# Performance work log

Measured on AMD Instinct MI355X. Metric: run time of the kernel, lower is better.

The kernel has to match this reference:

```python
import jax, jax.numpy as jnp
import numpy as np

B = 8
FEAT = 256
HID = 256
NCLS = 80
SIZES = [(128, 128), (64, 64), (32, 32), (16, 16), (8, 8)]
DELTA_XY = 0.1   # dd_delta_range_xy
DELTA_WH = 2.0   # dd_delta_range_wh
PRIOR_P = 0.01   # prior_cls_prob


def _priors():
    # prior_cxcy: normalized grid centers per pyramid level (sine_pos_encodings id maps,
    # normalize=True with all-ones masks). prior_wh: (1/fW, 1/fH) per level.
    cxcy, wh = [], []
    for (h, w) in SIZES:
        cy = (jnp.arange(h, dtype=jnp.float32) + 0.5) / h
        cx = (jnp.arange(w, dtype=jnp.float32) + 0.5) / w
        gx, gy = jnp.meshgrid(cx, cy, indexing='xy')           # [h, w]
        cxcy.append(jnp.stack([gx, gy], axis=-1).reshape(h * w, 2))
        wh.append(jnp.broadcast_to(jnp.array([1.0 / w, 1.0 / h], jnp.float32), (h * w, 2)))
    return jnp.concatenate(cxcy, axis=0), jnp.concatenate(wh, axis=0)  # [N,2], [N,2]


def _mlp(x, Wh, bh, Wo, bo):
    # Linear(feat->hidden) + ReLU, then Linear(hidden->out)
    h = jax.nn.relu(jnp.einsum('bnf,hf->bnh', x, Wh) + bh)
    return jnp.einsum('bnh,oh->bno', h, Wo) + bo


def setup_inputs() -> dict:
    key = jax.random.key(0)
    ks = jax.random.split(key, 12)
    inp = {}
    for i, (h, w) in enumerate(SIZES):
        inp[f'fm{i}'] = jax.random.normal(ks[i], (B, FEAT, h, w), dtype=jnp.float32)
    s_in = 1.0 / np.sqrt(FEAT)
    s_h = 1.0 / np.sqrt(HID)
    bias_value = float(-np.log((1.0 - PRIOR_P) / PRIOR_P))
    inp['cls_Wh'] = jax.random.normal(ks[5], (HID, FEAT), dtype=jnp.float32) * s_in
    inp['cls_bh'] = jnp.zeros((HID,), jnp.float32)
    inp['cls_Wo'] = jax.random.normal(ks[6], (NCLS, HID), dtype=jnp.float32) * s_h
    inp['cls_bo'] = jnp.full((NCLS,), bias_value, jnp.float32)  # focal prior bias init
    inp['box_Wh'] = jax.random.normal(ks[7], (HID, FEAT), dtype=jnp.float32) * s_in
    inp['box_bh'] = jnp.zeros((HID,), jnp.float32)
    inp['box_Wo'] = jax.random.normal(ks[8], (4, HID), dtype=jnp.float32) * s_h
    inp['box_bo'] = jnp.zeros((4,), jnp.float32)  # zero-init box bias
    return inp


def reference(fm0, fm1, fm2, fm3, fm4,
              cls_Wh, cls_bh, cls_Wo, cls_bo,
              box_Wh, box_bh, box_Wo, box_bo):
    fms = [fm0, fm1, fm2, fm3, fm4]
    # obj_feats: concat of flatten(2).permute(0,2,1) -> [B, N, FEAT]
    obj_feats = jnp.concatenate(
        [f.reshape(B, FEAT, -1).transpose(0, 2, 1) for f in fms], axis=1)
    cls_logits = _mlp(obj_feats, cls_Wh, cls_bh, cls_Wo, cls_bo)   # [B, N, NCLS]
    box_logits = _mlp(obj_feats, box_Wh, box_bh, box_Wo, box_bo)   # [B, N, 4]
    box_deltas = jnp.tanh(box_logits)
    prior_cxcy, prior_wh = _priors()
    pred_cxcy = prior_cxcy[None] + DELTA_XY * box_deltas[:, :, :2]
    pred_wh = prior_wh[None] * (DELTA_WH ** box_deltas[:, :, 2:])
    # pack [cls_logits | pred_boxes(cxcywh)] -> [B, N, NCLS+4]
    return jnp.concatenate([cls_logits, pred_cxcy, pred_wh], axis=-1)
```

## Files before the change

kernel.cpp:

```cpp
#include <hip/hip_runtime.h>
#include <hip/hip_bf16.h>
#include <math.h>
#include <stdint.h>

#define NTOK 21824

typedef __attribute__((ext_vector_type(8)))  short bf16x8;
typedef __attribute__((ext_vector_type(4)))  float f32x4;
typedef __attribute__((ext_vector_type(16))) float f32x16;

__device__ __forceinline__ uint32_t f2bf(float f) {
    uint32_t u = __builtin_bit_cast(uint32_t, f);
    return (u + 0x7FFFu + ((u >> 16) & 1u)) >> 16;
}
__device__ __forceinline__ uint32_t pkbf2(float lo, float hi) {
    __hip_bfloat162 h = __float22bfloat162_rn(float2{lo, hi});
    uint32_t r; __builtin_memcpy(&r, &h, 4);
    return r;
}

#define WOFF_CWH 0
#define WOFF_BWH 65536
#define WOFF_CWO 131072
#define WOFF_BWO 151552

__global__ void prep_weights(const float* __restrict__ cWh, const float* __restrict__ cWo,
                             const float* __restrict__ bWh, const float* __restrict__ bWo,
                             uint16_t* __restrict__ ws) {
    int i = blockIdx.x * 256 + threadIdx.x;
    if (i >= 155648) return;
    uint32_t v;
    if (i < 65536)       v = f2bf(cWh[i]);
    else if (i < 131072) v = f2bf(bWh[i - 65536]);
    else if (i < 151552) v = f2bf(cWo[i - 131072]);
    else { int j = i - 151552; v = (j < 1024) ? f2bf(bWo[j]) : 0u; }
    ws[i] = (uint16_t)v;
}

__global__ __launch_bounds__(512, 4) void dfd_fused(
    const float* __restrict__ fm0, const float* __restrict__ fm1,
    const float* __restrict__ fm2, const float* __restrict__ fm3,
    const float* __restrict__ fm4,
    const float* __restrict__ cls_bh, const float* __restrict__ cls_bo,
    const float* __restrict__ box_bh, const float* __restrict__ box_bo,
    const uint16_t* __restrict__ wbf,
    float* __restrict__ out)
{
    __shared__ uint16_t LB[64 * 512];
    uint16_t* Xs = LB;
    uint16_t* Hs = LB;

    const int tid  = threadIdx.x;
    const int lane = tid & 63;
    const int w    = tid >> 6;
    const int r    = lane & 15;
    const int q    = lane >> 4;
    const int col  = lane & 31;
    const int hi   = lane >> 5;
    const int n0   = blockIdx.x * 64;
    const int b    = blockIdx.y;

    const float* fm; int off, ls;
    if      (n0 < 16384) { fm = fm0; off = 0;     ls = 7; }
    else if (n0 < 20480) { fm = fm1; off = 16384; ls = 6; }
    else if (n0 < 21504) { fm = fm2; off = 20480; ls = 5; }
    else if (n0 < 21760) { fm = fm3; off = 21504; ls = 4; }
    else                 { fm = fm4; off = 21760; ls = 3; }
    const int dim = 1 << ls;
    const int hw  = dim * dim;
    const int p0  = n0 - off;

    {
        const int t  = lane;
        const int sw = (t & 7) << 3;
        const float* src = fm + (size_t)b * 256 * hw + p0 + t;
        #pragma unroll
        for (int i = 0; i < 4; ++i) {
            const int f0 = w * 8 + i * 64;
            float x[8];
            #pragma unroll
            for (int e = 0; e < 8; ++e) x[e] = src[(size_t)(f0 + e) * hw];
            uint4 pk;
            pk.x = pkbf2(x[0], x[1]); pk.y = pkbf2(x[2], x[3]);
            pk.z = pkbf2(x[4], x[5]); pk.w = pkbf2(x[6], x[7]);
            *reinterpret_cast<uint4*>(&Xs[t * 256 + (f0 ^ sw)]) = pk;
        }
    }
    __syncthreads();

    f32x16 acc[2][2];
    {
        #pragma unroll
        for (int mt = 0; mt < 2; ++mt)
            #pragma unroll
            for (int nt = 0; nt < 2; ++nt)
                #pragma unroll
                for (int e = 0; e < 16; ++e) acc[mt][nt][e] = 0.f;

        const int hh0 = w * 64;
        const uint16_t* Wbase = (w < 4) ? wbf + WOFF_CWH + hh0 * 256
                                        : wbf + WOFF_BWH + (hh0 - 256) * 256;
        const int kh = hi * 8;
        const uint16_t* Wr = Wbase + col * 256 + kh;
        const int sw0 = (col & 7) << 3;

        #pragma unroll
        for (int ks = 0; ks < 16; ++ks) {
            const bf16x8 a0 = *(const bf16x8*)(Wr + ks * 16);
            const bf16x8 a1 = *(const bf16x8*)(Wr + 8192 + ks * 16);
            const int kx = (ks * 16 + kh) ^ sw0;
            const bf16x8 x0 = *(const bf16x8*)&Xs[col * 256 + kx];
            const bf16x8 x1 = *(const bf16x8*)&Xs[(32 + col) * 256 + kx];
            acc[0][0] = __builtin_amdgcn_mfma_f32_32x32x16_bf16(a0, x0, acc[0][0], 0, 0, 0);
            acc[0][1] = __builtin_amdgcn_mfma_f32_32x32x16_bf16(a0, x1, acc[0][1], 0, 0, 0);
            acc[1][0] = __builtin_amdgcn_mfma_f32_32x32x16_bf16(a1, x0, acc[1][0], 0, 0, 0);
            acc[1][1] = __builtin_amdgcn_mfma_f32_32x32x16_bf16(a1, x1, acc[1][1], 0, 0, 0);
        }
    }
    __syncthreads();

    {
        const int hh0 = w * 64;
        const float* bh_ = (w < 4) ? cls_bh + hh0 : box_bh + (hh0 - 256);
        #pragma unroll
        for (int mt = 0; mt < 2; ++mt) {
            #pragma unroll
            for (int nt = 0; nt < 2; ++nt) {
                const int t   = nt * 32 + col;
                const int swt = (t & 7) << 3;
                #pragma unroll
                for (int g = 0; g < 4; ++g) {
                    const int hb = mt * 32 + 8 * g + 4 * hi;
                    const f32x4 bv = *(const f32x4*)(bh_ + hb);
                    const float v0 = fmaxf(acc[mt][nt][4 * g + 0] + bv[0], 0.f);
                    const float v1 = fmaxf(acc[mt][nt][4 * g + 1] + bv[1], 0.f);
                    const float v2 = fmaxf(acc[mt][nt][4 * g + 2] + bv[2], 0.f);
                    const float v3 = fmaxf(acc[mt][nt][4 * g + 3] + bv[3], 0.f);
                    uint2 pk; pk.x = pkbf2(v0, v1); pk.y = pkbf2(v2, v3);
                    *reinterpret_cast<uint2*>(&Hs[t * 512 + ((hh0 + hb) ^ swt)]) = pk;
                }
            }
        }
    }
    __syncthreads();

    if (w < 5) {
        f32x4 c[4];
        #pragma unroll
        for (int m = 0; m < 4; ++m) c[m] = {0.f, 0.f, 0.f, 0.f};
        const uint16_t* Bw = wbf + WOFF_CWO + (w * 16 + r) * 256 + q * 8;
        #pragma unroll
        for (int kq = 0; kq < 8; ++kq) {
            const bf16x8 bfr = *(const bf16x8*)(Bw + kq * 32);
            #pragma unroll
            for (int m = 0; m < 4; ++m) {
                const int t = m * 16 + r;
                const int kcol = (kq * 32 + q * 8) ^ ((t & 7) << 3);
                const bf16x8 a = *(const bf16x8*)&Hs[t * 512 + kcol];
                c[m] = __builtin_amdgcn_mfma_f32_16x16x32_bf16(a, bfr, c[m], 0, 0, 0);
            }
        }
        const float bo_l = cls_bo[w * 16 + r];
        #pragma unroll
        for (int m = 0; m < 4; ++m)
            #pragma unroll
            for (int jj = 0; jj < 4; ++jj)
                out[((size_t)b * NTOK + n0 + m * 16 + q * 4 + jj) * 84 + w * 16 + r]
                    = c[m][jj] + bo_l;
    } else if (w < 7) {
        const int m0 = (w - 5) * 2;
        f32x4 c[2];
        c[0] = {0.f, 0.f, 0.f, 0.f}; c[1] = {0.f, 0.f, 0.f, 0.f};
        const uint16_t* Bw = wbf + WOFF_BWO + r * 256 + q * 8;
        #pragma unroll
        for (int kq = 0; kq < 8; ++kq) {
            const bf16x8 bfr = *(const bf16x8*)(Bw + kq * 32);
            #pragma unroll
            for (int mm = 0; mm < 2; ++mm) {
                const int t = (m0 + mm) * 16 + r;
                const int kcol = 256 + ((kq * 32 + q * 8) ^ ((t & 7) << 3));
                const bf16x8 a = *(const bf16x8*)&Hs[t * 512 + kcol];
                c[mm] = __builtin_amdgcn_mfma_f32_16x16x32_bf16(a, bfr, c[mm], 0, 0, 0);
            }
        }
        if (r < 4) {
            const float bo_l = box_bo[r];
            const float inv  = 1.0f / (float)dim;
            #pragma unroll
            for (int mm = 0; mm < 2; ++mm)
                #pragma unroll
                for (int jj = 0; jj < 4; ++jj) {
                    const int t = (m0 + mm) * 16 + q * 4 + jj;
                    const int p = p0 + t;
                    const float d = tanhf(c[mm][jj] + bo_l);
                    float val;
                    if (r == 0)      val = ((float)(p & (dim - 1)) + 0.5f) * inv + 0.1f * d;
                    else if (r == 1) val = ((float)(p >> ls) + 0.5f) * inv + 0.1f * d;
                    else             val = exp2f(d) * inv;
                    out[((size_t)b * NTOK + n0 + t) * 84 + 80 + r] = val;
                }
        }
    }
}

extern "C" void kernel_launch(void* const* d_in, const int* in_sizes, int n_in,
                              void* d_out, int out_size, void* d_ws, size_t ws_size,
                              hipStream_t stream) {
    uint16_t* ws = (uint16_t*)d_ws;
    prep_weights<<<608, 256, 0, stream>>>(
        (const float*)d_in[5],  (const float*)d_in[7],
        (const float*)d_in[9],  (const float*)d_in[11], ws);
    dim3 grid(NTOK / 64, 8);
    dfd_fused<<<grid, 512, 0, stream>>>(
        (const float*)d_in[0], (const float*)d_in[1], (const float*)d_in[2],
        (const float*)d_in[3], (const float*)d_in[4],
        (const float*)d_in[6],  (const float*)d_in[8],
        (const float*)d_in[10], (const float*)d_in[12],
        ws, (float*)d_out);
}
```

Measured before the change: 135.7 us.

## Split fused MLP into two kernels with bf16 hidden buffer in workspace

```diff
diff --git a/kernel.cpp b/kernel.cpp
--- a/kernel.cpp
+++ b/kernel.cpp
@@ -23,6 +23,7 @@
 #define WOFF_BWH 65536
 #define WOFF_CWO 131072
 #define WOFF_BWO 151552
+#define HID_OFF  155648
 
 __global__ void prep_weights(const float* __restrict__ cWh, const float* __restrict__ cWo,
                              const float* __restrict__ bWh, const float* __restrict__ bWo,
@@ -35,6 +36,178 @@
     else if (i < 151552) v = f2bf(cWo[i - 131072]);
     else { int j = i - 151552; v = (j < 1024) ? f2bf(bWo[j]) : 0u; }
     ws[i] = (uint16_t)v;
+}
+
+__device__ __forceinline__ void level_lookup(
+    int n0, const float* fm0, const float* fm1, const float* fm2,
+    const float* fm3, const float* fm4, const float*& fm, int& off, int& ls) {
+    if      (n0 < 16384) { fm = fm0; off = 0;     ls = 7; }
+    else if (n0 < 20480) { fm = fm1; off = 16384; ls = 6; }
+    else if (n0 < 21504) { fm = fm2; off = 20480; ls = 5; }
+    else if (n0 < 21760) { fm = fm3; off = 21504; ls = 4; }
+    else                 { fm = fm4; off = 21760; ls = 3; }
+}
+
+__global__ __launch_bounds__(512, 4) void dfd_g1(
+    const float* __restrict__ fm0, const float* __restrict__ fm1,
+    const float* __restrict__ fm2, const float* __restrict__ fm3,
+    const float* __restrict__ fm4,
+    const float* __restrict__ cls_bh, const float* __restrict__ box_bh,
+    const uint16_t* __restrict__ wbf,
+    uint16_t* __restrict__ hid,
+    int b0)
+{
+    __shared__ uint16_t Xs[64 * 256];
+
+    const int tid  = threadIdx.x;
+    const int lane = tid & 63;
+    const int w    = tid >> 6;
+    const int col  = lane & 31;
+    const int hi   = lane >> 5;
+    const int n0   = blockIdx.x * 64;
+    const int lb   = blockIdx.y;
+    const int b    = b0 + lb;
+
+    const float* fm; int off, ls;
+    level_lookup(n0, fm0, fm1, fm2, fm3, fm4, fm, off, ls);
+    const int hw = 1 << (2 * ls);
+    const int p0 = n0 - off;
+
+    {
+        const int t  = lane;
+        const int sw = (t & 7) << 3;
+        const float* src = fm + (size_t)b * 256 * hw + p0 + t;
+        #pragma unroll
+        for (int i = 0; i < 4; ++i) {
+            const int f0 = w * 8 + i * 64;
+            float x[8];
+            #pragma unroll
+            for (int e = 0; e < 8; ++e) x[e] = src[(size_t)(f0 + e) * hw];
+            uint4 pk;
+            pk.x = pkbf2(x[0], x[1]); pk.y = pkbf2(x[2], x[3]);
+            pk.z = pkbf2(x[4], x[5]); pk.w = pkbf2(x[6], x[7]);
+            *reinterpret_cast<uint4*>(&Xs[t * 256 + (f0 ^ sw)]) = pk;
+        }
+    }
+    __syncthreads();
+
+    f32x16 acc[2][2];
+    #pragma unroll
+    for (int mt = 0; mt < 2; ++mt)
+        #pragma unroll
+        for (int nt = 0; nt < 2; ++nt)
+            #pragma unroll
+            for (int e = 0; e < 16; ++e) acc[mt][nt][e] = 0.f;
+
+    const int hh0 = w * 64;
+    const uint16_t* Wbase = (w < 4) ? wbf + WOFF_CWH + hh0 * 256
+                                    : wbf + WOFF_BWH + (hh0 - 256) * 256;
+    const int kh = hi * 8;
+    const uint16_t* Wr = Wbase + col * 256 + kh;
+    const int sw0 = (col & 7) << 3;
+
+    #pragma unroll
+    for (int ks = 0; ks < 16; ++ks) {
+        const bf16x8 a0 = *(const bf16x8*)(Wr + ks * 16);
+        const bf16x8 a1 = *(const bf16x8*)(Wr + 8192 + ks * 16);
+        const int kx = (ks * 16 + kh) ^ sw0;
+        const bf16x8 x0 = *(const bf16x8*)&Xs[col * 256 + kx];
+        const bf16x8 x1 = *(const bf16x8*)&Xs[(32 + col) * 256 + kx];
+        acc[0][0] = __builtin_amdgcn_mfma_f32_32x32x16_bf16(a0, x0, acc[0][0], 0, 0, 0);
+        acc[0][1] = __builtin_amdgcn_mfma_f32_32x32x16_bf16(a0, x1, acc[0][1], 0, 0, 0);
+        acc[1][0] = __builtin_amdgcn_mfma_f32_32x32x16_bf16(a1, x0, acc[1][0], 0, 0, 0);
+        acc[1][1] = __builtin_amdgcn_mfma_f32_32x32x16_bf16(a1, x1, acc[1][1], 0, 0, 0);
+    }
+
+    const float* bh_ = (w < 4) ? cls_bh + hh0 : box_bh + (hh0 - 256);
+    #pragma unroll
+    for (int nt = 0; nt < 2; ++nt) {
+        const int t = nt * 32 + col;
+        uint16_t* hrow = hid + ((size_t)lb * NTOK + n0 + t) * 512 + hh0;
+        #pragma unroll
+        for (int mt = 0; mt < 2; ++mt) {
+            #pragma unroll
+            for (int g = 0; g < 4; ++g) {
+                const int hb = mt * 32 + 8 * g + 4 * hi;
+                const f32x4 bv = *(const f32x4*)(bh_ + hb);
+                const float v0 = fmaxf(acc[mt][nt][4 * g + 0] + bv[0], 0.f);
+                const float v1 = fmaxf(acc[mt][nt][4 * g + 1] + bv[1], 0.f);
+                const float v2 = fmaxf(acc[mt][nt][4 * g + 2] + bv[2], 0.f);
+                const float v3 = fmaxf(acc[mt][nt][4 * g + 3] + bv[3], 0.f);
+                uint2 pk; pk.x = pkbf2(v0, v1); pk.y = pkbf2(v2, v3);
+                *reinterpret_cast<uint2*>(hrow + hb) = pk;
+            }
+        }
+    }
+}
+
+__global__ __launch_bounds__(256, 6) void dfd_g2(
+    const float* __restrict__ cls_bo, const float* __restrict__ box_bo,
+    const uint16_t* __restrict__ wbf,
+    const uint16_t* __restrict__ hid,
+    float* __restrict__ out,
+    int b0)
+{
+    const int tid  = threadIdx.x;
+    const int lane = tid & 63;
+    const int w    = tid >> 6;
+    const int r    = lane & 15;
+    const int q    = lane >> 4;
+    const int n0   = blockIdx.x * 64;
+    const int lb   = blockIdx.y;
+    const int b    = b0 + lb;
+    const int t0   = n0 + w * 16;
+
+    int off, ls; const float* fm_unused;
+    level_lookup(n0, nullptr, nullptr, nullptr, nullptr, nullptr, fm_unused, off, ls);
+    const int dim = 1 << ls;
+    const int p0  = n0 - off;
+
+    f32x4 c[6];
+    #pragma unroll
+    for (int m = 0; m < 6; ++m) c[m] = {0.f, 0.f, 0.f, 0.f};
+
+    const uint16_t* hrow = hid + ((size_t)lb * NTOK + t0 + r) * 512 + q * 8;
+    const uint16_t* WoA  = wbf + WOFF_CWO + r * 256 + q * 8;
+    const uint16_t* WoB  = wbf + WOFF_BWO + r * 256 + q * 8;
+
+    #pragma unroll
+    for (int kq = 0; kq < 8; ++kq) {
+        const bf16x8 hbc = *(const bf16x8*)(hrow + kq * 32);
+        const bf16x8 hbb = *(const bf16x8*)(hrow + 256 + kq * 32);
+        #pragma unroll
+        for (int m = 0; m < 5; ++m) {
+            const bf16x8 a = *(const bf16x8*)(WoA + m * 4096 + kq * 32);
+            c[m] = __builtin_amdgcn_mfma_f32_16x16x32_bf16(a, hbc, c[m], 0, 0, 0);
+        }
+        const bf16x8 ab = *(const bf16x8*)(WoB + kq * 32);
+        c[5] = __builtin_amdgcn_mfma_f32_16x16x32_bf16(ab, hbb, c[5], 0, 0, 0);
+    }
+
+    float* orow = out + ((size_t)b * NTOK + t0 + r) * 84;
+    #pragma unroll
+    for (int m = 0; m < 5; ++m) {
+        const f32x4 bo = *(const f32x4*)(cls_bo + m * 16 + q * 4);
+        f32x4 v;
+        #pragma unroll
+        for (int jj = 0; jj < 4; ++jj) v[jj] = c[m][jj] + bo[jj];
+        *(f32x4*)(orow + m * 16 + q * 4) = v;
+    }
+    if (q == 0) {
+        const f32x4 bo = *(const f32x4*)box_bo;
+        const float inv = 1.0f / (float)dim;
+        const int p = p0 + w * 16 + r;
+        const float d0 = tanhf(c[5][0] + bo[0]);
+        const float d1 = tanhf(c[5][1] + bo[1]);
+        const float d2 = tanhf(c[5][2] + bo[2]);
+        const float d3 = tanhf(c[5][3] + bo[3]);
+        f32x4 v;
+        v[0] = ((float)(p & (dim - 1)) + 0.5f) * inv + 0.1f * d0;
+        v[1] = ((float)(p >> ls) + 0.5f) * inv + 0.1f * d1;
+        v[2] = exp2f(d2) * inv;
+        v[3] = exp2f(d3) * inv;
+        *(f32x4*)(orow + 80) = v;
+    }
 }
 
 __global__ __launch_bounds__(512, 4) void dfd_fused(
@@ -61,13 +234,9 @@
     const int b    = blockIdx.y;
 
     const float* fm; int off, ls;
-    if      (n0 < 16384) { fm = fm0; off = 0;     ls = 7; }
-    else if (n0 < 20480) { fm = fm1; off = 16384; ls = 6; }
-    else if (n0 < 21504) { fm = fm2; off = 20480; ls = 5; }
-    else if (n0 < 21760) { fm = fm3; off = 21504; ls = 4; }
-    else                 { fm = fm4; off = 21760; ls = 3; }
+    level_lookup(n0, fm0, fm1, fm2, fm3, fm4, fm, off, ls);
     const int dim = 1 << ls;
-    const int hw  = dim * dim;
+    const int hw  = 1 << (2 * ls);
     const int p0  = n0 - off;
 
     {
@@ -210,11 +379,34 @@
     prep_weights<<<608, 256, 0, stream>>>(
         (const float*)d_in[5],  (const float*)d_in[7],
         (const float*)d_in[9],  (const float*)d_in[11], ws);
-    dim3 grid(NTOK / 64, 8);
-    dfd_fused<<<grid, 512, 0, stream>>>(
-        (const float*)d_in[0], (const float*)d_in[1], (const float*)d_in[2],
-        (const float*)d_in[3], (const float*)d_in[4],
-        (const float*)d_in[6],  (const float*)d_in[8],
-        (const float*)d_in[10], (const float*)d_in[12],
-        ws, (float*)d_out);
-}
+
+    const size_t HID_B_PER_BATCH = (size_t)NTOK * 512 * 2;
+    const size_t W_BYTES = (size_t)HID_OFF * 2;
+    int nb = 0;
+    if      (ws_size >= W_BYTES + 4 * HID_B_PER_BATCH) nb = 4;
+    else if (ws_size >= W_BYTES + 2 * HID_B_PER_BATCH) nb = 2;
+    else if (ws_size >= W_BYTES + 1 * HID_B_PER_BATCH) nb = 1;
+
+    if (nb > 0) {
+        uint16_t* hid = ws + HID_OFF;
+        for (int b0 = 0; b0 < 8; b0 += nb) {
+            dim3 g(NTOK / 64, nb);
+            dfd_g1<<<g, 512, 0, stream>>>(
+                (const float*)d_in[0], (const float*)d_in[1], (const float*)d_in[2],
+                (const float*)d_in[3], (const float*)d_in[4],
+                (const float*)d_in[6], (const float*)d_in[10],
+                ws, hid, b0);
+            dfd_g2<<<g, 256, 0, stream>>>(
+                (const float*)d_in[8], (const float*)d_in[12],
+                ws, hid, (float*)d_out, b0);
+        }
+    } else {
+        dim3 grid(NTOK / 64, 8);
+        dfd_fused<<<grid, 512, 0, stream>>>(
+            (const float*)d_in[0], (const float*)d_in[1], (const float*)d_in[2],
+            (const float*)d_in[3], (const float*)d_in[4],
+            (const float*)d_in[6],  (const float*)d_in[8],
+            (const float*)d_in[10], (const float*)d_in[12],
+            ws, (float*)d_out);
+    }
+}
```

After: 290.6 us (median of 2 runs). 2.14x slower.

## Halve token tile to 32 with 4-wave blocks and rebalance second-layer work

Applied to the files above, without the earlier changes.

```diff
diff --git a/kernel.cpp b/kernel.cpp
--- a/kernel.cpp
+++ b/kernel.cpp
@@ -37,7 +37,7 @@
     ws[i] = (uint16_t)v;
 }
 
-__global__ __launch_bounds__(512, 4) void dfd_fused(
+__global__ __launch_bounds__(256, 4) void dfd_fused(
     const float* __restrict__ fm0, const float* __restrict__ fm1,
     const float* __restrict__ fm2, const float* __restrict__ fm3,
     const float* __restrict__ fm4,
@@ -46,7 +46,7 @@
     const uint16_t* __restrict__ wbf,
     float* __restrict__ out)
 {
-    __shared__ uint16_t LB[64 * 512];
+    __shared__ uint16_t LB[32 * 512];
     uint16_t* Xs = LB;
     uint16_t* Hs = LB;
 
@@ -57,7 +57,7 @@
     const int q    = lane >> 4;
     const int col  = lane & 31;
     const int hi   = lane >> 5;
-    const int n0   = blockIdx.x * 64;
+    const int n0   = blockIdx.x * 32;
     const int b    = blockIdx.y;
 
     const float* fm; int off, ls;
@@ -67,16 +67,17 @@
     else if (n0 < 21760) { fm = fm3; off = 21504; ls = 4; }
     else                 { fm = fm4; off = 21760; ls = 3; }
     const int dim = 1 << ls;
-    const int hw  = dim * dim;
+    const int hw  = 1 << (2 * ls);
     const int p0  = n0 - off;
 
     {
-        const int t  = lane;
+        const int t  = tid & 31;
+        const int fg = tid >> 5;
         const int sw = (t & 7) << 3;
         const float* src = fm + (size_t)b * 256 * hw + p0 + t;
         #pragma unroll
         for (int i = 0; i < 4; ++i) {
-            const int f0 = w * 8 + i * 64;
+            const int f0 = fg * 32 + i * 8;
             float x[8];
             #pragma unroll
             for (int e = 0; e < 8; ++e) x[e] = src[(size_t)(f0 + e) * hw];
@@ -88,117 +89,110 @@
     }
     __syncthreads();
 
-    f32x16 acc[2][2];
-    {
-        #pragma unroll
-        for (int mt = 0; mt < 2; ++mt)
-            #pragma unroll
-            for (int nt = 0; nt < 2; ++nt)
-                #pragma unroll
-                for (int e = 0; e < 16; ++e) acc[mt][nt][e] = 0.f;
-
-        const int hh0 = w * 64;
-        const uint16_t* Wbase = (w < 4) ? wbf + WOFF_CWH + hh0 * 256
-                                        : wbf + WOFF_BWH + (hh0 - 256) * 256;
+    f32x16 acc[4];
+    {
+        #pragma unroll
+        for (int mt = 0; mt < 4; ++mt)
+            #pragma unroll
+            for (int e = 0; e < 16; ++e) acc[mt][e] = 0.f;
+
+        const uint16_t* Wbase = (w < 2) ? wbf + WOFF_CWH + (w * 128) * 256
+                                        : wbf + WOFF_BWH + ((w - 2) * 128) * 256;
         const int kh = hi * 8;
         const uint16_t* Wr = Wbase + col * 256 + kh;
         const int sw0 = (col & 7) << 3;
 
         #pragma unroll
         for (int ks = 0; ks < 16; ++ks) {
-            const bf16x8 a0 = *(const bf16x8*)(Wr + ks * 16);
-            const bf16x8 a1 = *(const bf16x8*)(Wr + 8192 + ks * 16);
             const int kx = (ks * 16 + kh) ^ sw0;
             const bf16x8 x0 = *(const bf16x8*)&Xs[col * 256 + kx];
-            const bf16x8 x1 = *(const bf16x8*)&Xs[(32 + col) * 256 + kx];
-            acc[0][0] = __builtin_amdgcn_mfma_f32_32x32x16_bf16(a0, x0, acc[0][0], 0, 0, 0);
-            acc[0][1] = __builtin_amdgcn_mfma_f32_32x32x16_bf16(a0, x1, acc[0][1], 0, 0, 0);
-            acc[1][0] = __builtin_amdgcn_mfma_f32_32x32x16_bf16(a1, x0, acc[1][0], 0, 0, 0);
-            acc[1][1] = __builtin_amdgcn_mfma_f32_32x32x16_bf16(a1, x1, acc[1][1], 0, 0, 0);
+            #pragma unroll
+            for (int mt = 0; mt < 4; ++mt) {
+                const bf16x8 a = *(const bf16x8*)(Wr + mt * 8192 + ks * 16);
+                acc[mt] = __builtin_amdgcn_mfma_f32_32x32x16_bf16(a, x0, acc[mt], 0, 0, 0);
+            }
         }
     }
     __syncthreads();
 
     {
-        const int hh0 = w * 64;
-        const float* bh_ = (w < 4) ? cls_bh + hh0 : box_bh + (hh0 - 256);
-        #pragma unroll
-        for (int mt = 0; mt < 2; ++mt) {
-            #pragma unroll
-            for (int nt = 0; nt < 2; ++nt) {
-                const int t   = nt * 32 + col;
-                const int swt = (t & 7) << 3;
+        const float* bh_ = (w < 2) ? cls_bh + w * 128 : box_bh + (w - 2) * 128;
+        const int t   = col;
+        const int swt = (t & 7) << 3;
+        #pragma unroll
+        for (int mt = 0; mt < 4; ++mt) {
+            #pragma unroll
+            for (int g = 0; g < 4; ++g) {
+                const int hb = mt * 32 + 8 * g + 4 * hi;
+                const f32x4 bv = *(const f32x4*)(bh_ + hb);
+                const float v0 = fmaxf(acc[mt][4 * g + 0] + bv[0], 0.f);
+                const float v1 = fmaxf(acc[mt][4 * g + 1] + bv[1], 0.f);
+                const float v2 = fmaxf(acc[mt][4 * g + 2] + bv[2], 0.f);
+                const float v3 = fmaxf(acc[mt][4 * g + 3] + bv[3], 0.f);
+                uint2 pk; pk.x = pkbf2(v0, v1); pk.y = pkbf2(v2, v3);
+                *reinterpret_cast<uint2*>(&Hs[t * 512 + ((w * 128 + hb) ^ swt)]) = pk;
+            }
+        }
+    }
+    __syncthreads();
+
+    {
+        const int th = w & 1;
+        const int ms = w >> 1;
+        const int t  = th * 16 + r;
+        const int swt = (r & 7) << 3;
+        const uint16_t* hrow = &Hs[t * 512];
+        const int m0 = ms * 3;
+
+        f32x4 c[3];
+        c[0] = {0.f,0.f,0.f,0.f}; c[1] = {0.f,0.f,0.f,0.f}; c[2] = {0.f,0.f,0.f,0.f};
+        const uint16_t* WoA = wbf + WOFF_CWO + r * 256 + q * 8;
+        const uint16_t* WoB = wbf + WOFF_BWO + r * 256 + q * 8;
+
+        #pragma unroll
+        for (int kq = 0; kq < 8; ++kq) {
+            const int kcol = (kq * 32 + q * 8) ^ swt;
+            const bf16x8 a = *(const bf16x8*)&hrow[kcol];
+            const bf16x8 b0 = *(const bf16x8*)(WoA + (m0 + 0) * 4096 + kq * 32);
+            const bf16x8 b1 = *(const bf16x8*)(WoA + (m0 + 1) * 4096 + kq * 32);
+            c[0] = __builtin_amdgcn_mfma_f32_16x16x32_bf16(a, b0, c[0], 0, 0, 0);
+            c[1] = __builtin_amdgcn_mfma_f32_16x16x32_bf16(a, b1, c[1], 0, 0, 0);
+            if (ms == 0) {
+                const bf16x8 b2 = *(const bf16x8*)(WoA + 2 * 4096 + kq * 32);
+                c[2] = __builtin_amdgcn_mfma_f32_16x16x32_bf16(a, b2, c[2], 0, 0, 0);
+            } else {
+                const bf16x8 ab = *(const bf16x8*)&hrow[256 + kcol];
+                const bf16x8 b2 = *(const bf16x8*)(WoB + kq * 32);
+                c[2] = __builtin_amdgcn_mfma_f32_16x16x32_bf16(ab, b2, c[2], 0, 0, 0);
+            }
+        }
+
+        const int ncls = (ms == 0) ? 3 : 2;
+        #pragma unroll
+        for (int i = 0; i < 3; ++i) {
+            if (i < ncls) {
+                const int m = m0 + i;
+                const float bo_l = cls_bo[m * 16 + r];
                 #pragma unroll
-                for (int g = 0; g < 4; ++g) {
-                    const int hb = mt * 32 + 8 * g + 4 * hi;
-                    const f32x4 bv = *(const f32x4*)(bh_ + hb);
-                    const float v0 = fmaxf(acc[mt][nt][4 * g + 0] + bv[0], 0.f);
-                    const float v1 = fmaxf(acc[mt][nt][4 * g + 1] + bv[1], 0.f);
-                    const float v2 = fmaxf(acc[mt][nt][4 * g + 2] + bv[2], 0.f);
-                    const float v3 = fmaxf(acc[mt][nt][4 * g + 3] + bv[3], 0.f);
-                    uint2 pk; pk.x = pkbf2(v0, v1); pk.y = pkbf2(v2, v3);
-                    *reinterpret_cast<uint2*>(&Hs[t * 512 + ((hh0 + hb) ^ swt)]) = pk;
-                }
-            }
-        }
-    }
-    __syncthreads();
-
-    if (w < 5) {
-        f32x4 c[4];
-        #pragma unroll
-        for (int m = 0; m < 4; ++m) c[m] = {0.f, 0.f, 0.f, 0.f};
-        const uint16_t* Bw = wbf + WOFF_CWO + (w * 16 + r) * 256 + q * 8;
-        #pragma unroll
-        for (int kq = 0; kq < 8; ++kq) {
-            const bf16x8 bfr = *(const bf16x8*)(Bw + kq * 32);
-            #pragma unroll
-            for (int m = 0; m < 4; ++m) {
-                const int t = m * 16 + r;
-                const int kcol = (kq * 32 + q * 8) ^ ((t & 7) << 3);
-                const bf16x8 a = *(const bf16x8*)&Hs[t * 512 + kcol];
-                c[m] = __builtin_amdgcn_mfma_f32_16x16x32_bf16(a, bfr, c[m], 0, 0, 0);
-            }
-        }
-        const float bo_l = cls_bo[w * 16 + r];
-        #pragma unroll
-        for (int m = 0; m < 4; ++m)
-            #pragma unroll
-            for (int jj = 0; jj < 4; ++jj)
-                out[((size_t)b * NTOK + n0 + m * 16 + q * 4 + jj) * 84 + w * 16 + r]
-                    = c[m][jj] + bo_l;
-    } else if (w < 7) {
-        const int m0 = (w - 5) * 2;
-        f32x4 c[2];
-        c[0] = {0.f, 0.f, 0.f, 0.f}; c[1] = {0.f, 0.f, 0.f, 0.f};
-        const uint16_t* Bw = wbf + WOFF_BWO + r * 256 + q * 8;
-        #pragma unroll
-        for (int kq = 0; kq < 8; ++kq) {
-            const bf16x8 bfr = *(const bf16x8*)(Bw + kq * 32);
-            #pragma unroll
-            for (int mm = 0; mm < 2; ++mm) {
-                const int t = (m0 + mm) * 16 + r;
-                const int kcol = 256 + ((kq * 32 + q * 8) ^ ((t & 7) << 3));
-                const bf16x8 a = *(const bf16x8*)&Hs[t * 512 + kcol];
-                c[mm] = __builtin_amdgcn_mfma_f32_16x16x32_bf16(a, bfr, c[mm], 0, 0, 0);
-            }
-        }
-        if (r < 4) {
+                for (int jj = 0; jj < 4; ++jj)
+                    out[((size_t)b * NTOK + n0 + th * 16 + q * 4 + jj) * 84 + m * 16 + r]
+                        = c[i][jj] + bo_l;
+            }
+        }
+        if (ms == 1 && r < 4) {
             const float bo_l = box_bo[r];
             const float inv  = 1.0f / (float)dim;
             #pragma unroll
-            for (int mm = 0; mm < 2; ++mm)
-                #pragma unroll
-                for (int jj = 0; jj < 4; ++jj) {
-                    const int t = (m0 + mm) * 16 + q * 4 + jj;
-                    const int p = p0 + t;
-                    const float d = tanhf(c[mm][jj] + bo_l);
-                    float val;
-                    if (r == 0)      val = ((float)(p & (dim - 1)) + 0.5f) * inv + 0.1f * d;
-                    else if (r == 1) val = ((float)(p >> ls) + 0.5f) * inv + 0.1f * d;
-                    else             val = exp2f(d) * inv;
-                    out[((size_t)b * NTOK + n0 + t) * 84 + 80 + r] = val;
-                }
+            for (int jj = 0; jj < 4; ++jj) {
+                const int t2 = th * 16 + q * 4 + jj;
+                const int p  = p0 + t2;
+                const float d = tanhf(c[2][jj] + bo_l);
+                float val;
+                if (r == 0)      val = ((float)(p & (dim - 1)) + 0.5f) * inv + 0.1f * d;
+                else if (r == 1) val = ((float)(p >> ls) + 0.5f) * inv + 0.1f * d;
+                else             val = exp2f(d) * inv;
+                out[((size_t)b * NTOK + n0 + t2) * 84 + 80 + r] = val;
+            }
         }
     }
 }
@@ -210,8 +204,8 @@
     prep_weights<<<608, 256, 0, stream>>>(
         (const float*)d_in[5],  (const float*)d_in[7],
         (const float*)d_in[9],  (const float*)d_in[11], ws);
-    dim3 grid(NTOK / 64, 8);
-    dfd_fused<<<grid, 512, 0, stream>>>(
+    dim3 grid(NTOK / 32, 8);
+    dfd_fused<<<grid, 256, 0, stream>>>(
         (const float*)d_in[0], (const float*)d_in[1], (const float*)d_in[2],
         (const float*)d_in[3], (const float*)d_in[4],
         (const float*)d_in[6],  (const float*)d_in[8],
```

Result: slower. 263.2 us (+94.0%).

## Split cls and box heads across blocks with 128-token tiles

Applied to the files above, without the earlier changes.

```diff
diff --git a/kernel.cpp b/kernel.cpp
--- a/kernel.cpp
+++ b/kernel.cpp
@@ -4,6 +4,7 @@
 #include <stdint.h>
 
 #define NTOK 21824
+#define NTILE128 171
 
 typedef __attribute__((ext_vector_type(8)))  short bf16x8;
 typedef __attribute__((ext_vector_type(4)))  float f32x4;
@@ -37,7 +38,7 @@
     ws[i] = (uint16_t)v;
 }
 
-__global__ __launch_bounds__(512, 4) void dfd_fused(
+__global__ __launch_bounds__(512, 4) void dfd_head(
     const float* __restrict__ fm0, const float* __restrict__ fm1,
     const float* __restrict__ fm2, const float* __restrict__ fm3,
     const float* __restrict__ fm4,
@@ -46,7 +47,13 @@
     const uint16_t* __restrict__ wbf,
     float* __restrict__ out)
 {
-    __shared__ uint16_t LB[64 * 512];
+    const int g    = blockIdx.x;
+    const int s    = g & 15;
+    const int tile = (g >> 4) * 8 + (s & 7);
+    const int head = s >> 3;
+    if (tile >= NTILE128) return;
+
+    __shared__ uint16_t LB[128 * 256];
     uint16_t* Xs = LB;
     uint16_t* Hs = LB;
 
@@ -57,7 +64,7 @@
     const int q    = lane >> 4;
     const int col  = lane & 31;
     const int hi   = lane >> 5;
-    const int n0   = blockIdx.x * 64;
+    const int n0   = tile * 128;
     const int b    = blockIdx.y;
 
     const float* fm; int off, ls;
@@ -67,138 +74,134 @@
     else if (n0 < 21760) { fm = fm3; off = 21504; ls = 4; }
     else                 { fm = fm4; off = 21760; ls = 3; }
     const int dim = 1 << ls;
-    const int hw  = dim * dim;
+    const int hw  = 1 << (2 * ls);
     const int p0  = n0 - off;
+    const int T   = (n0 == 21760) ? 64 : 128;
+    const int NT16 = T >> 4;
 
     {
-        const int t  = lane;
+        const int t  = tid & 127;
+        const int fg = tid >> 7;
         const int sw = (t & 7) << 3;
-        const float* src = fm + (size_t)b * 256 * hw + p0 + t;
-        #pragma unroll
-        for (int i = 0; i < 4; ++i) {
-            const int f0 = w * 8 + i * 64;
-            float x[8];
-            #pragma unroll
-            for (int e = 0; e < 8; ++e) x[e] = src[(size_t)(f0 + e) * hw];
-            uint4 pk;
-            pk.x = pkbf2(x[0], x[1]); pk.y = pkbf2(x[2], x[3]);
-            pk.z = pkbf2(x[4], x[5]); pk.w = pkbf2(x[6], x[7]);
-            *reinterpret_cast<uint4*>(&Xs[t * 256 + (f0 ^ sw)]) = pk;
+        if (t < T) {
+            const float* src = fm + (size_t)b * 256 * hw + p0 + t;
+            #pragma unroll
+            for (int i = 0; i < 8; ++i) {
+                const int f0 = fg * 64 + i * 8;
+                float x[8];
+                #pragma unroll
+                for (int e = 0; e < 8; ++e) x[e] = src[(size_t)(f0 + e) * hw];
+                uint4 pk;
+                pk.x = pkbf2(x[0], x[1]); pk.y = pkbf2(x[2], x[3]);
+                pk.z = pkbf2(x[4], x[5]); pk.w = pkbf2(x[6], x[7]);
+                *reinterpret_cast<uint4*>(&Xs[t * 256 + (f0 ^ sw)]) = pk;
+            }
         }
     }
     __syncthreads();
 
-    f32x16 acc[2][2];
+    f32x16 acc[4];
     {
         #pragma unroll
-        for (int mt = 0; mt < 2; ++mt)
-            #pragma unroll
-            for (int nt = 0; nt < 2; ++nt)
-                #pragma unroll
-                for (int e = 0; e < 16; ++e) acc[mt][nt][e] = 0.f;
-
-        const int hh0 = w * 64;
-        const uint16_t* Wbase = (w < 4) ? wbf + WOFF_CWH + hh0 * 256
-                                        : wbf + WOFF_BWH + (hh0 - 256) * 256;
+        for (int nt = 0; nt < 4; ++nt)
+            #pragma unroll
+            for (int e = 0; e < 16; ++e) acc[nt][e] = 0.f;
+
+        const int hhw = w * 32;
+        const uint16_t* Wbase = wbf + (head ? WOFF_BWH : WOFF_CWH) + hhw * 256;
         const int kh = hi * 8;
         const uint16_t* Wr = Wbase + col * 256 + kh;
         const int sw0 = (col & 7) << 3;
 
         #pragma unroll
         for (int ks = 0; ks < 16; ++ks) {
-            const bf16x8 a0 = *(const bf16x8*)(Wr + ks * 16);
-            const bf16x8 a1 = *(const bf16x8*)(Wr + 8192 + ks * 16);
+            const bf16x8 a = *(const bf16x8*)(Wr + ks * 16);
             const int kx = (ks * 16 + kh) ^ sw0;
-            const bf16x8 x0 = *(const bf16x8*)&Xs[col * 256 + kx];
-            const bf16x8 x1 = *(const bf16x8*)&Xs[(32 + col) * 256 + kx];
-            acc[0][0] = __builtin_amdgcn_mfma_f32_32x32x16_bf16(a0, x0, acc[0][0], 0, 0, 0);
-            acc[0][1] = __builtin_amdgcn_mfma_f32_32x32x16_bf16(a0, x1, acc[0][1], 0, 0, 0);
-            acc[1][0] = __builtin_amdgcn_mfma_f32_32x32x16_bf16(a1, x0, acc[1][0], 0, 0, 0);
-            acc[1][1] = __builtin_amdgcn_mfma_f32_32x32x16_bf16(a1, x1, acc[1][1], 0, 0, 0);
+            #pragma unroll
+            for (int nt = 0; nt < 4; ++nt) {
+                const bf16x8 x = *(const bf16x8*)&Xs[(nt * 32 + col) * 256 + kx];
+                acc[nt] = __builtin_amdgcn_mfma_f32_32x32x16_bf16(a, x, acc[nt], 0, 0, 0);
+            }
         }
     }
     __syncthreads();
 
     {
-        const int hh0 = w * 64;
-        const float* bh_ = (w < 4) ? cls_bh + hh0 : box_bh + (hh0 - 256);
+        const int hhw = w * 32;
+        const float* bh_ = (head ? box_bh : cls_bh) + hhw;
         #pragma unroll
-        for (int mt = 0; mt < 2; ++mt) {
-            #pragma unroll
-            for (int nt = 0; nt < 2; ++nt) {
-                const int t   = nt * 32 + col;
-                const int swt = (t & 7) << 3;
-                #pragma unroll
-                for (int g = 0; g < 4; ++g) {
-                    const int hb = mt * 32 + 8 * g + 4 * hi;
-                    const f32x4 bv = *(const f32x4*)(bh_ + hb);
-                    const float v0 = fmaxf(acc[mt][nt][4 * g + 0] + bv[0], 0.f);
-                    const float v1 = fmaxf(acc[mt][nt][4 * g + 1] + bv[1], 0.f);
-                    const float v2 = fmaxf(acc[mt][nt][4 * g + 2] + bv[2], 0.f);
-                    const float v3 = fmaxf(acc[mt][nt][4 * g + 3] + bv[3], 0.f);
-                    uint2 pk; pk.x = pkbf2(v0, v1); pk.y = pkbf2(v2, v3);
-                    *reinterpret_cast<uint2*>(&Hs[t * 512 + ((hh0 + hb) ^ swt)]) = pk;
+        for (int nt = 0; nt < 4; ++nt) {
+            const int t   = nt * 32 + col;
+            const int swt = (t & 7) << 3;
+            #pragma unroll
+            for (int g2 = 0; g2 < 4; ++g2) {
+                const int hb = 8 * g2 + 4 * hi;
+                const f32x4 bv = *(const f32x4*)(bh_ + hb);
+                const float v0 = fmaxf(acc[nt][4 * g2 + 0] + bv[0], 0.f);
+                const float v1 = fmaxf(acc[nt][4 * g2 + 1] + bv[1], 0.f);
+                const float v2 = fmaxf(acc[nt][4 * g2 + 2] + bv[2], 0.f);
+                const float v3 = fmaxf(acc[nt][4 * g2 + 3] + bv[3], 0.f);
+                uint2 pk; pk.x = pkbf2(v0, v1); pk.y = pkbf2(v2, v3);
+                *reinterpret_cast<uint2*>(&Hs[t * 256 + ((hhw + hb) ^ swt)]) = pk;
+            }
+        }
+    }
+    __syncthreads();
+
+    if (head == 0) {
+        if (w < 5) {
+            const uint16_t* Bw = wbf + WOFF_CWO + (w * 16 + r) * 256 + q * 8;
+            bf16x8 bfr[8];
+            #pragma unroll
+            for (int kq = 0; kq < 8; ++kq) bfr[kq] = *(const bf16x8*)(Bw + kq * 32);
+            const float bo_l = cls_bo[w * 16 + r];
+            #pragma unroll
+            for (int tt = 0; tt < 8; ++tt) {
+                if (tt < NT16) {
+                    const int tr  = tt * 16 + r;
+                    const int swt = (tr & 7) << 3;
+                    const uint16_t* hrow = &Hs[tr * 256];
+                    f32x4 c = {0.f, 0.f, 0.f, 0.f};
+                    #pragma unroll
+                    for (int kq = 0; kq < 8; ++kq) {
+                        const bf16x8 a = *(const bf16x8*)&hrow[(kq * 32 + q * 8) ^ swt];
+                        c = __builtin_amdgcn_mfma_f32_16x16x32_bf16(a, bfr[kq], c, 0, 0, 0);
+                    }
+                    #pragma unroll
+                    for (int jj = 0; jj < 4; ++jj)
+                        out[((size_t)b * NTOK + n0 + tt * 16 + q * 4 + jj) * 84 + w * 16 + r]
+                            = c[jj] + bo_l;
                 }
             }
         }
-    }
-    __syncthreads();
-
-    if (w < 5) {
-        f32x4 c[4];
-        #pragma unroll
-        for (int m = 0; m < 4; ++m) c[m] = {0.f, 0.f, 0.f, 0.f};
-        const uint16_t* Bw = wbf + WOFF_CWO + (w * 16 + r) * 256 + q * 8;
-        #pragma unroll
-        for (int kq = 0; kq < 8; ++kq) {
-            const bf16x8 bfr = *(const bf16x8*)(Bw + kq * 32);
-            #pragma unroll
-            for (int m = 0; m < 4; ++m) {
-                const int t = m * 16 + r;
-                const int kcol = (kq * 32 + q * 8) ^ ((t & 7) << 3);
-                const bf16x8 a = *(const bf16x8*)&Hs[t * 512 + kcol];
-                c[m] = __builtin_amdgcn_mfma_f32_16x16x32_bf16(a, bfr, c[m], 0, 0, 0);
-            }
-        }
-        const float bo_l = cls_bo[w * 16 + r];
-        #pragma unroll
-        for (int m = 0; m < 4; ++m)
-            #pragma unroll
-            for (int jj = 0; jj < 4; ++jj)
-                out[((size_t)b * NTOK + n0 + m * 16 + q * 4 + jj) * 84 + w * 16 + r]
-                    = c[m][jj] + bo_l;
-    } else if (w < 7) {
-        const int m0 = (w - 5) * 2;
-        f32x4 c[2];
-        c[0] = {0.f, 0.f, 0.f, 0.f}; c[1] = {0.f, 0.f, 0.f, 0.f};
-        const uint16_t* Bw = wbf + WOFF_BWO + r * 256 + q * 8;
-        #pragma unroll
-        for (int kq = 0; kq < 8; ++kq) {
-            const bf16x8 bfr = *(const bf16x8*)(Bw + kq * 32);
-            #pragma unroll
-            for (int mm = 0; mm < 2; ++mm) {
-                const int t = (m0 + mm) * 16 + r;
-                const int kcol = 256 + ((kq * 32 + q * 8) ^ ((t & 7) << 3));
-                const bf16x8 a = *(const bf16x8*)&Hs[t * 512 + kcol];
-                c[mm] = __builtin_amdgcn_mfma_f32_16x16x32_bf16(a, bfr, c[mm], 0, 0, 0);
-            }
-        }
-        if (r < 4) {
-            const float bo_l = box_bo[r];
-            const float inv  = 1.0f / (float)dim;
-            #pragma unroll
-            for (int mm = 0; mm < 2; ++mm)
+    } else {
+        if (w < NT16) {
+            const uint16_t* Bw = wbf + WOFF_BWO + r * 256 + q * 8;
+            const int tr  = w * 16 + r;
+            const int swt = (tr & 7) << 3;
+            const uint16_t* hrow = &Hs[tr * 256];
+            f32x4 c = {0.f, 0.f, 0.f, 0.f};
+            #pragma unroll
+            for (int kq = 0; kq < 8; ++kq) {
+                const bf16x8 a   = *(const bf16x8*)&hrow[(kq * 32 + q * 8) ^ swt];
+                const bf16x8 bfr = *(const bf16x8*)(Bw + kq * 32);
+                c = __builtin_amdgcn_mfma_f32_16x16x32_bf16(a, bfr, c, 0, 0, 0);
+            }
+            if (r < 4) {
+                const float bo_l = box_bo[r];
+                const float inv  = 1.0f / (float)dim;
                 #pragma unroll
                 for (int jj = 0; jj < 4; ++jj) {
-                    const int t = (m0 + mm) * 16 + q * 4 + jj;
-                    const int p = p0 + t;
-                    const float d = tanhf(c[mm][jj] + bo_l);
+                    const int t2 = w * 16 + q * 4 + jj;
+                    const int p  = p0 + t2;
+                    const float d = tanhf(c[jj] + bo_l);
                     float val;
                     if (r == 0)      val = ((float)(p & (dim - 1)) + 0.5f) * inv + 0.1f * d;
                     else if (r == 1) val = ((float)(p >> ls) + 0.5f) * inv + 0.1f * d;
                     else             val = exp2f(d) * inv;
-                    out[((size_t)b * NTOK + n0 + t) * 84 + 80 + r] = val;
+                    out[((size_t)b * NTOK + n0 + t2) * 84 + 80 + r] = val;
                 }
+            }
         }
     }
 }
@@ -210,8 +213,8 @@
     prep_weights<<<608, 256, 0, stream>>>(
         (const float*)d_in[5],  (const float*)d_in[7],
         (const float*)d_in[9],  (const float*)d_in[11], ws);
-    dim3 grid(NTOK / 64, 8);
-    dfd_fused<<<grid, 512, 0, stream>>>(
+    dim3 grid(22 * 16, 8);
+    dfd_head<<<grid, 512, 0, stream>>>(
         (const float*)d_in[0], (const float*)d_in[1], (const float*)d_in[2],
         (const float*)d_in[3], (const float*)d_in[4],
         (const float*)d_in[6],  (const float*)d_in[8],
```

Result: faster. 111.6 us (-17.8%).
